# Kernel tuning notes

Measured on AMD Instinct MI355X. Metric: run time of the kernel, lower is better.

The kernel has to match this reference:

```python
import jax, jax.numpy as jnp
import numpy as np

R = 256        # reservoir_size
M = 256        # samples
S = 512        # steps
D = 2          # n_features (dims)
B = 16         # bits_per_feature
LUT_LEN = 18   # 2**18 LUT entries per node; >= max possible state index
OUT = 32       # output_size


def _first_primes(n):
    lim = 2000  # p_256 = 1619 < 2000
    is_p = np.ones(lim, dtype=bool)
    is_p[:2] = False
    for i in range(2, int(lim ** 0.5) + 1):
        if is_p[i]:
            is_p[i * i::i] = False
    return np.nonzero(is_p)[0][:n].astype(np.int32)


def setup_inputs() -> dict:
    key = jax.random.key(0)
    k = jax.random.split(key, 6)
    x = jax.random.randint(k[0], (M, S, D, B), 0, 2).astype(bool)
    lut = jax.random.randint(k[1], (R, 2 ** LUT_LEN), 0, 2).astype(jnp.int32)
    init_res = jax.random.randint(k[2], (R,), 0, 2).astype(bool)
    W = jax.random.randint(k[3], (R, R), 0, 2).astype(bool)
    primes = jnp.asarray(_first_primes(R))  # first R primes, like primes[:reservoir_size]
    input_nodes = jax.random.permutation(k[4], R)[: D * B]  # randperm(R)[:b*d]
    readout_w = jax.random.normal(k[5], (OUT, R), jnp.float32) * (1.0 / np.sqrt(R))
    readout_b = jnp.zeros((OUT,), jnp.float32)
    return dict(x=x, lut=lut, init_res=init_res, W=W, primes=primes,
                input_nodes=input_nodes, readout_w=readout_w, readout_b=readout_b)


def reference(x, lut, init_res, W, primes, input_nodes, readout_w, readout_b):
    m, s, d, b = x.shape
    r = init_res.shape[0]
    xs = x.reshape(m, s, d * b).transpose(1, 0, 2)  # [s, m, nb] time-major for scan
    Wi = W.astype(jnp.int32)                        # [R, R]
    node_idx = jnp.arange(r)                        # [R]

    def step(res, xt):
        # 1. write encoded input bits into the reservoir (scatter)
        res = res.at[:, input_nodes].set(xt)                    # [m, R] bool
        # 2. state_idx[n] = sum_k res[k] * primes[k] * W[n, k]  (primes-weighted masked sum)
        v = res.astype(jnp.int32) * primes                      # [m, R]
        state_idx = v @ Wi.T                                    # [m, R] int32
        # 3. per-node LUT gather -> next boolean state
        res = lut[node_idx[None, :], state_idx].astype(bool)    # [m, R]
        return res, None

    res0 = jnp.broadcast_to(init_res, (m, r))  # every sample starts from initial_reservoir
    res_final, _ = jax.lax.scan(step, res0, xs)
    # readout on final reservoir state
    return res_final.astype(jnp.float32) @ readout_w.T + readout_b  # [m, OUT]
```

## Files before the change

### kernel.cpp

```cpp
#include <hip/hip_runtime.h>
#include <hip/hip_fp16.h>

#define RES 256
#define MS 256
#define ST 512
#define NB 32
#define LUTLEN 262144
#define LUTW 8192
#define NOUT 32
#define NBLK 256

typedef __attribute__((ext_vector_type(8))) _Float16 half8;
typedef __attribute__((ext_vector_type(4))) float f32x4;

__global__ __launch_bounds__(256) void lut_offsets_kernel(const int* __restrict__ W,
                                                          const int* __restrict__ primes,
                                                          int* __restrict__ off) {
    __shared__ int s[RES];
    const int n = threadIdx.x;
    int maxsum = 0;
    for (int k = 0; k < RES; ++k)
        maxsum += (W[n * RES + k] != 0) ? primes[k] : 0;
    int nw = (maxsum >> 5) + 1;
    s[n] = nw;
    __syncthreads();
    for (int d = 1; d < RES; d <<= 1) {
        int v = (n >= d) ? s[n - d] : 0;
        __syncthreads();
        s[n] += v;
        __syncthreads();
    }
    off[n] = s[n] - nw;
    if (n == RES - 1) off[RES] = s[n];
}

__global__ __launch_bounds__(512) void pack_lut2_kernel(const int* __restrict__ lut,
                                                        const int* __restrict__ off,
                                                        unsigned* __restrict__ lutp) {
    const int n = blockIdx.x;
    const int o = off[n];
    const int nw = off[n + 1] - o;
    const int* src = lut + (size_t)n * LUTLEN;
    for (int w = threadIdx.x; w < nw; w += blockDim.x) {
        const int4* p = (const int4*)(src + (size_t)w * 32);
        unsigned word = 0u;
#pragma unroll
        for (int c = 0; c < 8; ++c) {
            const int4 v = p[c];
            word |= (v.x != 0 ? 1u : 0u) << (4 * c + 0);
            word |= (v.y != 0 ? 1u : 0u) << (4 * c + 1);
            word |= (v.z != 0 ? 1u : 0u) << (4 * c + 2);
            word |= (v.w != 0 ? 1u : 0u) << (4 * c + 3);
        }
        lutp[o + w] = word;
    }
}

__global__ __launch_bounds__(256) void pack_x_kernel(const int* __restrict__ x,
                                                     unsigned* __restrict__ xp) {
    const int total = MS * ST;
    int w = blockIdx.x * blockDim.x + threadIdx.x;
    const int stride = gridDim.x * blockDim.x;
    for (; w < total; w += stride) {
        const int4* p = (const int4*)(x + (size_t)w * 32);
        unsigned word = 0u;
#pragma unroll
        for (int c = 0; c < 8; ++c) {
            const int4 v = p[c];
            word |= (v.x != 0 ? 1u : 0u) << (4 * c + 0);
            word |= (v.y != 0 ? 1u : 0u) << (4 * c + 1);
            word |= (v.z != 0 ? 1u : 0u) << (4 * c + 2);
            word |= (v.w != 0 ? 1u : 0u) << (4 * c + 3);
        }
        const int m = w >> 9;
        const int t = w & (ST - 1);
        xp[t * MS + m] = word;
    }
}

template<bool LP, bool XP>
__global__ __launch_bounds__(512) void reservoir_kernel(
    const int* __restrict__ xraw,
    const unsigned* __restrict__ xp,
    const int* __restrict__ lutraw,
    const unsigned* __restrict__ lutp,
    const int* __restrict__ off,
    const int* __restrict__ init_res,
    const int* __restrict__ W,
    const int* __restrict__ primes,
    const int* __restrict__ input_nodes,
    const float* __restrict__ rw,
    const float* __restrict__ rb,
    float* __restrict__ out)
{
    __shared__ __align__(16) _Float16 vArow[2][264];
    __shared__ unsigned xw_lds[ST];

    const int tid = threadIdx.x;
    const int lane = tid & 63;
    const int wid = tid >> 6;
    const int g = lane >> 4;
    const int r = lane & 15;
    const int m0 = blockIdx.x;

    const int n0 = wid * 32 + r;
    const int n1 = wid * 32 + 16 + r;

    const _Float16 p0 = (_Float16)(float)primes[n0];
    const _Float16 p1 = (_Float16)(float)primes[n1];
    const _Float16 z  = (_Float16)0.0f;

    const int off0 = LP ? off[n0] : 0;
    const int off1 = LP ? off[n1] : 0;

    int j0 = -1, j1 = -1;
    for (int j = 0; j < NB; ++j) {
        int nn = input_nodes[j];
        if (nn == n0) j0 = j;
        if (nn == n1) j1 = j;
    }

    half8 B0[8], B1[8];
#pragma unroll
    for (int kc = 0; kc < 8; ++kc) {
        const int kb = kc * 32 + g * 8;
        const int4* w0p = (const int4*)(W + n0 * RES + kb);
        const int4* w1p = (const int4*)(W + n1 * RES + kb);
        const int4 wa = w0p[0], wb = w0p[1], wc = w1p[0], wd = w1p[1];
        half8 b0, b1;
        b0[0] = wa.x != 0 ? (_Float16)1.0f : z;  b0[1] = wa.y != 0 ? (_Float16)1.0f : z;
        b0[2] = wa.z != 0 ? (_Float16)1.0f : z;  b0[3] = wa.w != 0 ? (_Float16)1.0f : z;
        b0[4] = wb.x != 0 ? (_Float16)1.0f : z;  b0[5] = wb.y != 0 ? (_Float16)1.0f : z;
        b0[6] = wb.z != 0 ? (_Float16)1.0f : z;  b0[7] = wb.w != 0 ? (_Float16)1.0f : z;
        b1[0] = wc.x != 0 ? (_Float16)1.0f : z;  b1[1] = wc.y != 0 ? (_Float16)1.0f : z;
        b1[2] = wc.z != 0 ? (_Float16)1.0f : z;  b1[3] = wc.w != 0 ? (_Float16)1.0f : z;
        b1[4] = wd.x != 0 ? (_Float16)1.0f : z;  b1[5] = wd.y != 0 ? (_Float16)1.0f : z;
        b1[6] = wd.z != 0 ? (_Float16)1.0f : z;  b1[7] = wd.w != 0 ? (_Float16)1.0f : z;
        B0[kc] = b0; B1[kc] = b1;
    }

    if (XP) xw_lds[tid] = xp[tid * MS + m0];

    if (g == 0) {
        int b0, b1;
        if (XP) {
            const unsigned xa = xp[m0];
            b0 = (j0 >= 0) ? (int)((xa >> j0) & 1u) : (init_res[n0] != 0);
            b1 = (j1 >= 0) ? (int)((xa >> j1) & 1u) : (init_res[n1] != 0);
        } else {
            b0 = (j0 >= 0) ? (xraw[(m0 * ST) * NB + j0] != 0) : (init_res[n0] != 0);
            b1 = (j1 >= 0) ? (xraw[(m0 * ST) * NB + j1] != 0) : (init_res[n1] != 0);
        }
        vArow[0][n0] = b0 ? p0 : z;
        vArow[0][n1] = b1 ? p1 : z;
    }
    __syncthreads();

#pragma unroll 1
    for (int t = 0; t < ST; ++t) {
        const int cur = t & 1, nxt = cur ^ 1;
        half8 A[8];
#pragma unroll
        for (int kc = 0; kc < 8; ++kc)
            A[kc] = *(const half8*)&vArow[cur][kc * 32 + g * 8];
        f32x4 c0a = {0.f,0.f,0.f,0.f}, c0b = {0.f,0.f,0.f,0.f};
        f32x4 c1a = {0.f,0.f,0.f,0.f}, c1b = {0.f,0.f,0.f,0.f};
#pragma unroll
        for (int kc = 0; kc < 8; kc += 2) {
            c0a = __builtin_amdgcn_mfma_f32_16x16x32_f16(A[kc],   B0[kc],   c0a, 0, 0, 0);
            c1a = __builtin_amdgcn_mfma_f32_16x16x32_f16(A[kc],   B1[kc],   c1a, 0, 0, 0);
            c0b = __builtin_amdgcn_mfma_f32_16x16x32_f16(A[kc+1], B0[kc+1], c0b, 0, 0, 0);
            c1b = __builtin_amdgcn_mfma_f32_16x16x32_f16(A[kc+1], B1[kc+1], c1b, 0, 0, 0);
        }

        if (g == 0) {
            const bool last = (t == ST - 1);
            const unsigned i0 = (unsigned)(c0a[0] + c0b[0]);
            const unsigned i1 = (unsigned)(c1a[0] + c1b[0]);
            unsigned w0, w1, s0, s1;
            if (LP) {
                w0 = lutp[off0 + (int)(i0 >> 5)];
                w1 = lutp[off1 + (int)(i1 >> 5)];
                s0 = i0 & 31u; s1 = i1 & 31u;
            } else {
                w0 = (unsigned)lutraw[(size_t)n0 * LUTLEN + i0];
                w1 = (unsigned)lutraw[(size_t)n1 * LUTLEN + i1];
                s0 = 0u; s1 = 0u;
            }
            int b0 = LP ? (int)((w0 >> s0) & 1u) : (w0 != 0u);
            int b1 = LP ? (int)((w1 >> s1) & 1u) : (w1 != 0u);
            if (!last) {
                if (XP) {
                    const unsigned xa = xw_lds[t + 1];
                    if (j0 >= 0) b0 = (int)((xa >> j0) & 1u);
                    if (j1 >= 0) b1 = (int)((xa >> j1) & 1u);
                } else {
                    if (j0 >= 0) b0 = (xraw[(m0 * ST + (t + 1)) * NB + j0] != 0);
                    if (j1 >= 0) b1 = (xraw[(m0 * ST + (t + 1)) * NB + j1] != 0);
                }
            }
            vArow[nxt][n0] = b0 ? p0 : z;
            vArow[nxt][n1] = b1 ? p1 : z;
        }
        __syncthreads();
    }

    if (tid < NOUT) {
        const int o = tid;
        float acc = rb[o];
        for (int n = 0; n < RES; ++n) {
            if (vArow[0][n] != z) acc += rw[o * RES + n];
        }
        out[m0 * NOUT + o] = acc;
    }
}

extern "C" void kernel_launch(void* const* d_in, const int* in_sizes, int n_in,
                              void* d_out, int out_size, void* d_ws, size_t ws_size,
                              hipStream_t stream) {
    const int* x           = (const int*)d_in[0];
    const int* lut         = (const int*)d_in[1];
    const int* init_res    = (const int*)d_in[2];
    const int* W           = (const int*)d_in[3];
    const int* primes      = (const int*)d_in[4];
    const int* input_nodes = (const int*)d_in[5];
    const float* rw        = (const float*)d_in[6];
    const float* rb        = (const float*)d_in[7];
    float* out = (float*)d_out;

    const size_t lutp_bytes = (size_t)RES * LUTW * sizeof(unsigned);
    const size_t xp_bytes   = (size_t)ST * MS * sizeof(unsigned);
    const size_t off_bytes  = (RES + 1) * sizeof(int);

    unsigned* lutp = nullptr;
    unsigned* xp = nullptr;
    int* off = nullptr;
    bool use_lp = false, use_xp = false;
    unsigned char* ws = (unsigned char*)d_ws;
    if (ws_size >= lutp_bytes + xp_bytes + 256 + off_bytes) {
        lutp = (unsigned*)ws;
        xp = (unsigned*)(ws + lutp_bytes);
        off = (int*)(ws + lutp_bytes + xp_bytes);
        use_lp = use_xp = true;
    } else if (ws_size >= xp_bytes) {
        xp = (unsigned*)ws;
        use_xp = true;
    }

    if (use_lp) {
        hipLaunchKernelGGL(lut_offsets_kernel, dim3(1), dim3(256), 0, stream, W, primes, off);
        hipLaunchKernelGGL(pack_lut2_kernel, dim3(RES), dim3(512), 0, stream, lut, off, lutp);
    }
    if (use_xp) hipLaunchKernelGGL(pack_x_kernel, dim3(512), dim3(256), 0, stream, x, xp);

    if (use_lp)
        hipLaunchKernelGGL((reservoir_kernel<true, true>), dim3(NBLK), dim3(512), 0, stream,
                           x, xp, lut, lutp, off, init_res, W, primes, input_nodes, rw, rb, out);
    else if (use_xp)
        hipLaunchKernelGGL((reservoir_kernel<false, true>), dim3(NBLK), dim3(512), 0, stream,
                           x, xp, lut, lutp, off, init_res, W, primes, input_nodes, rw, rb, out);
    else
        hipLaunchKernelGGL((reservoir_kernel<false, false>), dim3(NBLK), dim3(512), 0, stream,
                           x, xp, lut, lutp, off, init_res, W, primes, input_nodes, rw, rb, out);
}
```

Baseline: 410.5 us.

## Interleave two samples per block to hide LUT gather latency behind MFMA

Each block now processes two samples and software-pipelines them: while one sample's LUT gather is in flight, the other sample's MFMA state-index computation runs, and the results are finished after the opposite compute. The plain __syncthreads is replaced by an lgkmcnt wait plus s_barrier. This targets the serial latency chain of matmul, global gather and barrier per step. In exchange the grid is halved to 128 blocks, which lowers parallelism across CUs, and each thread holds more live state.

After: 659.9 us. 60.8% more time.

```diff
diff --git a/kernel.cpp b/kernel.cpp
--- a/kernel.cpp
+++ b/kernel.cpp
@@ -8,10 +8,16 @@
 #define LUTLEN 262144
 #define LUTW 8192
 #define NOUT 32
-#define NBLK 256
+#define SPB 2
+#define NBLK (MS / SPB)
 
 typedef __attribute__((ext_vector_type(8))) _Float16 half8;
 typedef __attribute__((ext_vector_type(4))) float f32x4;
+
+__device__ __forceinline__ void publish_barrier() {
+    asm volatile("s_waitcnt lgkmcnt(0)" ::: "memory");
+    __builtin_amdgcn_s_barrier();
+}
 
 __global__ __launch_bounds__(256) void lut_offsets_kernel(const int* __restrict__ W,
                                                           const int* __restrict__ primes,
@@ -93,15 +99,15 @@
     const float* __restrict__ rb,
     float* __restrict__ out)
 {
-    __shared__ __align__(16) _Float16 vArow[2][264];
-    __shared__ unsigned xw_lds[ST];
+    __shared__ __align__(16) _Float16 vA[2][2][264];
+    __shared__ unsigned xw_lds[2][ST];
 
     const int tid = threadIdx.x;
     const int lane = tid & 63;
     const int wid = tid >> 6;
     const int g = lane >> 4;
     const int r = lane & 15;
-    const int m0 = blockIdx.x;
+    const int m0 = blockIdx.x * SPB;
 
     const int n0 = wid * 32 + r;
     const int n1 = wid * 32 + 16 + r;
@@ -139,30 +145,37 @@
         B0[kc] = b0; B1[kc] = b1;
     }
 
-    if (XP) xw_lds[tid] = xp[tid * MS + m0];
+    if (XP) {
+        xw_lds[0][tid] = xp[tid * MS + m0];
+        xw_lds[1][tid] = xp[tid * MS + m0 + 1];
+    }
 
     if (g == 0) {
-        int b0, b1;
-        if (XP) {
-            const unsigned xa = xp[m0];
-            b0 = (j0 >= 0) ? (int)((xa >> j0) & 1u) : (init_res[n0] != 0);
-            b1 = (j1 >= 0) ? (int)((xa >> j1) & 1u) : (init_res[n1] != 0);
-        } else {
-            b0 = (j0 >= 0) ? (xraw[(m0 * ST) * NB + j0] != 0) : (init_res[n0] != 0);
-            b1 = (j1 >= 0) ? (xraw[(m0 * ST) * NB + j1] != 0) : (init_res[n1] != 0);
-        }
-        vArow[0][n0] = b0 ? p0 : z;
-        vArow[0][n1] = b1 ? p1 : z;
+#pragma unroll
+        for (int grp = 0; grp < 2; ++grp) {
+            const int sm = m0 + grp;
+            int b0, b1;
+            if (XP) {
+                const unsigned xa = xp[sm];
+                b0 = (j0 >= 0) ? (int)((xa >> j0) & 1u) : (init_res[n0] != 0);
+                b1 = (j1 >= 0) ? (int)((xa >> j1) & 1u) : (init_res[n1] != 0);
+            } else {
+                b0 = (j0 >= 0) ? (xraw[(sm * ST) * NB + j0] != 0) : (init_res[n0] != 0);
+                b1 = (j1 >= 0) ? (xraw[(sm * ST) * NB + j1] != 0) : (init_res[n1] != 0);
+            }
+            vA[grp][0][n0] = b0 ? p0 : z;
+            vA[grp][0][n1] = b1 ? p1 : z;
+        }
     }
     __syncthreads();
 
-#pragma unroll 1
-    for (int t = 0; t < ST; ++t) {
-        const int cur = t & 1, nxt = cur ^ 1;
+    auto COMPUTE = [&](int grp, int buf, int t,
+                       unsigned& w0, unsigned& w1, unsigned& s0, unsigned& s1,
+                       unsigned& xa) {
         half8 A[8];
 #pragma unroll
         for (int kc = 0; kc < 8; ++kc)
-            A[kc] = *(const half8*)&vArow[cur][kc * 32 + g * 8];
+            A[kc] = *(const half8*)&vA[grp][buf][kc * 32 + g * 8];
         f32x4 c0a = {0.f,0.f,0.f,0.f}, c0b = {0.f,0.f,0.f,0.f};
         f32x4 c1a = {0.f,0.f,0.f,0.f}, c1b = {0.f,0.f,0.f,0.f};
 #pragma unroll
@@ -172,12 +185,9 @@
             c0b = __builtin_amdgcn_mfma_f32_16x16x32_f16(A[kc+1], B0[kc+1], c0b, 0, 0, 0);
             c1b = __builtin_amdgcn_mfma_f32_16x16x32_f16(A[kc+1], B1[kc+1], c1b, 0, 0, 0);
         }
-
         if (g == 0) {
-            const bool last = (t == ST - 1);
             const unsigned i0 = (unsigned)(c0a[0] + c0b[0]);
             const unsigned i1 = (unsigned)(c1a[0] + c1b[0]);
-            unsigned w0, w1, s0, s1;
             if (LP) {
                 w0 = lutp[off0 + (int)(i0 >> 5)];
                 w1 = lutp[off1 + (int)(i1 >> 5)];
@@ -187,31 +197,63 @@
                 w1 = (unsigned)lutraw[(size_t)n1 * LUTLEN + i1];
                 s0 = 0u; s1 = 0u;
             }
+            xa = 0u;
+            if (t + 1 < ST) {
+                if (XP) xa = xw_lds[grp][t + 1];
+            }
+        }
+    };
+
+    auto FINISH = [&](int grp, int nbuf, int t,
+                      unsigned w0, unsigned w1, unsigned s0, unsigned s1,
+                      unsigned xa) {
+        if (g == 0) {
+            const bool last = (t == ST - 1);
             int b0 = LP ? (int)((w0 >> s0) & 1u) : (w0 != 0u);
             int b1 = LP ? (int)((w1 >> s1) & 1u) : (w1 != 0u);
             if (!last) {
                 if (XP) {
-                    const unsigned xa = xw_lds[t + 1];
                     if (j0 >= 0) b0 = (int)((xa >> j0) & 1u);
                     if (j1 >= 0) b1 = (int)((xa >> j1) & 1u);
                 } else {
-                    if (j0 >= 0) b0 = (xraw[(m0 * ST + (t + 1)) * NB + j0] != 0);
-                    if (j1 >= 0) b1 = (xraw[(m0 * ST + (t + 1)) * NB + j1] != 0);
+                    const int sm = m0 + grp;
+                    if (j0 >= 0) b0 = (xraw[(sm * ST + (t + 1)) * NB + j0] != 0);
+                    if (j1 >= 0) b1 = (xraw[(sm * ST + (t + 1)) * NB + j1] != 0);
                 }
             }
-            vArow[nxt][n0] = b0 ? p0 : z;
-            vArow[nxt][n1] = b1 ? p1 : z;
-        }
-        __syncthreads();
-    }
-
-    if (tid < NOUT) {
-        const int o = tid;
+            vA[grp][nbuf][n0] = b0 ? p0 : z;
+            vA[grp][nbuf][n1] = b1 ? p1 : z;
+        }
+    };
+
+    unsigned wA0, wA1, sA0, sA1, xaA;
+    unsigned wB0, wB1, sB0, sB1, xaB;
+
+    COMPUTE(0, 0, 0, wA0, wA1, sA0, sA1, xaA);
+#pragma unroll 1
+    for (int t = 0; t < ST - 1; ++t) {
+        const int cb = t & 1, nb = cb ^ 1;
+        COMPUTE(1, cb, t, wB0, wB1, sB0, sB1, xaB);
+        FINISH (0, nb, t, wA0, wA1, sA0, sA1, xaA);
+        publish_barrier();
+        COMPUTE(0, nb, t + 1, wA0, wA1, sA0, sA1, xaA);
+        FINISH (1, nb, t, wB0, wB1, sB0, sB1, xaB);
+        publish_barrier();
+    }
+    COMPUTE(1, 1, ST - 1, wB0, wB1, sB0, sB1, xaB);
+    FINISH (0, 0, ST - 1, wA0, wA1, sA0, sA1, xaA);
+    publish_barrier();
+    FINISH (1, 0, ST - 1, wB0, wB1, sB0, sB1, xaB);
+    publish_barrier();
+
+    if (tid < 2 * NOUT) {
+        const int grp = tid >> 5;
+        const int o = tid & 31;
         float acc = rb[o];
         for (int n = 0; n < RES; ++n) {
-            if (vArow[0][n] != z) acc += rw[o * RES + n];
-        }
-        out[m0 * NOUT + o] = acc;
+            if (vA[grp][0][n] != z) acc += rw[o * RES + n];
+        }
+        out[(m0 + grp) * NOUT + o] = acc;
     }
 }
 
```

## Spread LUT gathers over 32 lanes, split MFMA chains, and use a lighter barrier

Applied to the files above, without the earlier changes.

Each node's LUT lookup now runs on 32 lanes, one node per lane, instead of 16 lanes each doing two gathers, which halves the serial gather latency per wave. The MFMA accumulation is split into four independent chains per output for more instruction-level parallelism. The time loop is unrolled by two so the buffer indices are constants. __syncthreads is replaced by an LDS-only waitcnt plus s_barrier, and the next input word is read from LDS early in each step. The custom barrier relies on only LDS writes needing to be visible across threads.

Result: faster. 373.5 us (-9.0%).

```diff
diff --git a/kernel.cpp b/kernel.cpp
--- a/kernel.cpp
+++ b/kernel.cpp
@@ -12,6 +12,11 @@
 
 typedef __attribute__((ext_vector_type(8))) _Float16 half8;
 typedef __attribute__((ext_vector_type(4))) float f32x4;
+
+__device__ __forceinline__ void publish_barrier() {
+    asm volatile("s_waitcnt lgkmcnt(0)" ::: "memory");
+    __builtin_amdgcn_s_barrier();
+}
 
 __global__ __launch_bounds__(256) void lut_offsets_kernel(const int* __restrict__ W,
                                                           const int* __restrict__ primes,
@@ -103,22 +108,19 @@
     const int r = lane & 15;
     const int m0 = blockIdx.x;
 
+    const int nn = wid * 32 + (lane & 31);
+    const bool own = (lane < 32);
+
     const int n0 = wid * 32 + r;
-    const int n1 = wid * 32 + 16 + r;
-
-    const _Float16 p0 = (_Float16)(float)primes[n0];
-    const _Float16 p1 = (_Float16)(float)primes[n1];
+    const int n1 = n0 + 16;
+
+    const _Float16 pz = (_Float16)(float)primes[nn];
     const _Float16 z  = (_Float16)0.0f;
 
-    const int off0 = LP ? off[n0] : 0;
-    const int off1 = LP ? off[n1] : 0;
-
-    int j0 = -1, j1 = -1;
-    for (int j = 0; j < NB; ++j) {
-        int nn = input_nodes[j];
-        if (nn == n0) j0 = j;
-        if (nn == n1) j1 = j;
-    }
+    const unsigned* lpn = LP ? (lutp + off[nn]) : nullptr;
+    int jn = -1;
+    for (int j = 0; j < NB; ++j)
+        if (input_nodes[j] == nn) jn = j;
 
     half8 B0[8], B1[8];
 #pragma unroll
@@ -141,68 +143,71 @@
 
     if (XP) xw_lds[tid] = xp[tid * MS + m0];
 
-    if (g == 0) {
-        int b0, b1;
+    if (own) {
+        int b;
         if (XP) {
-            const unsigned xa = xp[m0];
-            b0 = (j0 >= 0) ? (int)((xa >> j0) & 1u) : (init_res[n0] != 0);
-            b1 = (j1 >= 0) ? (int)((xa >> j1) & 1u) : (init_res[n1] != 0);
+            const unsigned x0 = xp[m0];
+            b = (jn >= 0) ? (int)((x0 >> jn) & 1u) : (init_res[nn] != 0);
         } else {
-            b0 = (j0 >= 0) ? (xraw[(m0 * ST) * NB + j0] != 0) : (init_res[n0] != 0);
-            b1 = (j1 >= 0) ? (xraw[(m0 * ST) * NB + j1] != 0) : (init_res[n1] != 0);
-        }
-        vArow[0][n0] = b0 ? p0 : z;
-        vArow[0][n1] = b1 ? p1 : z;
+            b = (jn >= 0) ? (xraw[(m0 * ST) * NB + jn] != 0) : (init_res[nn] != 0);
+        }
+        vArow[0][nn] = b ? pz : z;
     }
     __syncthreads();
 
-#pragma unroll 1
-    for (int t = 0; t < ST; ++t) {
-        const int cur = t & 1, nxt = cur ^ 1;
+    auto STEP = [&](int cur, int nxt, int t) {
+        unsigned xa = 0u;
+        if (XP) xa = xw_lds[(t + 1) & (ST - 1)];
         half8 A[8];
 #pragma unroll
         for (int kc = 0; kc < 8; ++kc)
             A[kc] = *(const half8*)&vArow[cur][kc * 32 + g * 8];
-        f32x4 c0a = {0.f,0.f,0.f,0.f}, c0b = {0.f,0.f,0.f,0.f};
-        f32x4 c1a = {0.f,0.f,0.f,0.f}, c1b = {0.f,0.f,0.f,0.f};
-#pragma unroll
-        for (int kc = 0; kc < 8; kc += 2) {
-            c0a = __builtin_amdgcn_mfma_f32_16x16x32_f16(A[kc],   B0[kc],   c0a, 0, 0, 0);
-            c1a = __builtin_amdgcn_mfma_f32_16x16x32_f16(A[kc],   B1[kc],   c1a, 0, 0, 0);
-            c0b = __builtin_amdgcn_mfma_f32_16x16x32_f16(A[kc+1], B0[kc+1], c0b, 0, 0, 0);
-            c1b = __builtin_amdgcn_mfma_f32_16x16x32_f16(A[kc+1], B1[kc+1], c1b, 0, 0, 0);
-        }
-
-        if (g == 0) {
-            const bool last = (t == ST - 1);
-            const unsigned i0 = (unsigned)(c0a[0] + c0b[0]);
-            const unsigned i1 = (unsigned)(c1a[0] + c1b[0]);
-            unsigned w0, w1, s0, s1;
+        f32x4 a0 = {0.f,0.f,0.f,0.f}, a1 = {0.f,0.f,0.f,0.f};
+        f32x4 a2 = {0.f,0.f,0.f,0.f}, a3 = {0.f,0.f,0.f,0.f};
+        f32x4 b0 = {0.f,0.f,0.f,0.f}, b1 = {0.f,0.f,0.f,0.f};
+        f32x4 b2 = {0.f,0.f,0.f,0.f}, b3 = {0.f,0.f,0.f,0.f};
+        a0 = __builtin_amdgcn_mfma_f32_16x16x32_f16(A[0], B0[0], a0, 0, 0, 0);
+        b0 = __builtin_amdgcn_mfma_f32_16x16x32_f16(A[0], B1[0], b0, 0, 0, 0);
+        a1 = __builtin_amdgcn_mfma_f32_16x16x32_f16(A[1], B0[1], a1, 0, 0, 0);
+        b1 = __builtin_amdgcn_mfma_f32_16x16x32_f16(A[1], B1[1], b1, 0, 0, 0);
+        a2 = __builtin_amdgcn_mfma_f32_16x16x32_f16(A[2], B0[2], a2, 0, 0, 0);
+        b2 = __builtin_amdgcn_mfma_f32_16x16x32_f16(A[2], B1[2], b2, 0, 0, 0);
+        a3 = __builtin_amdgcn_mfma_f32_16x16x32_f16(A[3], B0[3], a3, 0, 0, 0);
+        b3 = __builtin_amdgcn_mfma_f32_16x16x32_f16(A[3], B1[3], b3, 0, 0, 0);
+        a0 = __builtin_amdgcn_mfma_f32_16x16x32_f16(A[4], B0[4], a0, 0, 0, 0);
+        b0 = __builtin_amdgcn_mfma_f32_16x16x32_f16(A[4], B1[4], b0, 0, 0, 0);
+        a1 = __builtin_amdgcn_mfma_f32_16x16x32_f16(A[5], B0[5], a1, 0, 0, 0);
+        b1 = __builtin_amdgcn_mfma_f32_16x16x32_f16(A[5], B1[5], b1, 0, 0, 0);
+        a2 = __builtin_amdgcn_mfma_f32_16x16x32_f16(A[6], B0[6], a2, 0, 0, 0);
+        b2 = __builtin_amdgcn_mfma_f32_16x16x32_f16(A[6], B1[6], b2, 0, 0, 0);
+        a3 = __builtin_amdgcn_mfma_f32_16x16x32_f16(A[7], B0[7], a3, 0, 0, 0);
+        b3 = __builtin_amdgcn_mfma_f32_16x16x32_f16(A[7], B1[7], b3, 0, 0, 0);
+
+        if (own) {
+            const float fa = (a0[0] + a1[0]) + (a2[0] + a3[0]);
+            const float fb = (b0[0] + b1[0]) + (b2[0] + b3[0]);
+            const float f = (g == 0) ? fa : fb;
+            const unsigned i = (unsigned)f;
+            int b;
             if (LP) {
-                w0 = lutp[off0 + (int)(i0 >> 5)];
-                w1 = lutp[off1 + (int)(i1 >> 5)];
-                s0 = i0 & 31u; s1 = i1 & 31u;
+                const unsigned w = lpn[i >> 5];
+                b = (int)((w >> (i & 31u)) & 1u);
             } else {
-                w0 = (unsigned)lutraw[(size_t)n0 * LUTLEN + i0];
-                w1 = (unsigned)lutraw[(size_t)n1 * LUTLEN + i1];
-                s0 = 0u; s1 = 0u;
+                b = (lutraw[(size_t)nn * LUTLEN + i] != 0);
             }
-            int b0 = LP ? (int)((w0 >> s0) & 1u) : (w0 != 0u);
-            int b1 = LP ? (int)((w1 >> s1) & 1u) : (w1 != 0u);
-            if (!last) {
-                if (XP) {
-                    const unsigned xa = xw_lds[t + 1];
-                    if (j0 >= 0) b0 = (int)((xa >> j0) & 1u);
-                    if (j1 >= 0) b1 = (int)((xa >> j1) & 1u);
-                } else {
-                    if (j0 >= 0) b0 = (xraw[(m0 * ST + (t + 1)) * NB + j0] != 0);
-                    if (j1 >= 0) b1 = (xraw[(m0 * ST + (t + 1)) * NB + j1] != 0);
-                }
+            if (t != ST - 1 && jn >= 0) {
+                b = XP ? (int)((xa >> jn) & 1u)
+                       : (xraw[(m0 * ST + t + 1) * NB + jn] != 0);
             }
-            vArow[nxt][n0] = b0 ? p0 : z;
-            vArow[nxt][n1] = b1 ? p1 : z;
-        }
-        __syncthreads();
+            vArow[nxt][nn] = b ? pz : z;
+        }
+        publish_barrier();
+    };
+
+#pragma unroll 1
+    for (int tt = 0; tt < ST; tt += 2) {
+        STEP(0, 1, tt);
+        STEP(1, 0, tt + 1);
     }
 
     if (tid < NOUT) {
```
